# Kernel tuning notes

Hardware: AMD Instinct MI355X
Metric: run time of the kernel (lower is better)

The kernel has to match this reference:

```python
import jax, jax.numpy as jnp
import numpy as np

PI = float(np.pi)


def _make_grid(H, W, stride, k, delta):
    """Gnomonic (tangent-plane) sampling grid for one spherical conv layer.
    Returns rows (Ho, K) and cols (Ho, Wo, K) of fractional pixel coords."""
    Ho, Wo = H // stride, W // stride
    j = jnp.arange(k, dtype=jnp.float32) - (k - 1) / 2.0
    t = jnp.tan(delta / k * j)                      # tangent-plane tap coords
    yy = jnp.repeat(t, k)                           # (K,) vertical
    xx = jnp.tile(t, k)                             # (K,) horizontal
    rho = jnp.sqrt(xx ** 2 + yy ** 2)
    rho_s = jnp.where(rho == 0, 1.0, rho)
    nu = jnp.arctan(rho)
    # latitude of each output row center (equirect: row -> colatitude)
    lat0 = PI / 2 - (jnp.arange(Ho, dtype=jnp.float32) * stride + 0.5) * (PI / H)
    sl, cl = jnp.sin(lat0)[:, None], jnp.cos(lat0)[:, None]   # (Ho,1)
    sn, cn = jnp.sin(nu)[None, :], jnp.cos(nu)[None, :]       # (1,K)
    lat = jnp.arcsin(jnp.clip(cn * sl + (yy[None, :] / rho_s[None, :]) * sn * cl, -1.0, 1.0))
    dlon = jnp.arctan2(xx[None, :] * sn, rho[None, :] * cl * cn - yy[None, :] * sl * sn)
    rows = (PI / 2 - lat) / PI * H - 0.5            # (Ho,K) fractional row
    dcol = dlon / (2 * PI) * W                      # (Ho,K) longitude offset in px
    cols = (jnp.arange(Wo, dtype=jnp.float32) * stride)[None, :, None] + dcol[:, None, :]
    return rows, cols


def _bilinear(x, rows, cols):
    """x: (B,C,H,W); rows (Ho,K); cols (Ho,Wo,K). Latitude clamped, longitude wrapped.
    Returns patches (B,C,Ho,Wo,K)."""
    B, C, H, W = x.shape
    r0 = jnp.floor(rows); wr = (rows - r0)[:, None, :]
    c0 = jnp.floor(cols); wc = cols - c0
    r0i = jnp.clip(r0, 0, H - 1).astype(jnp.int32)
    r1i = jnp.clip(r0 + 1, 0, H - 1).astype(jnp.int32)
    c0i = jnp.mod(c0.astype(jnp.int32), W)
    c1i = jnp.mod(c0i + 1, W)

    def g(ri, ci):
        return x[:, :, ri[:, None, :], ci]          # (B,C,Ho,Wo,K)

    return (g(r0i, c0i) * (1 - wr) * (1 - wc) + g(r0i, c1i) * (1 - wr) * wc
            + g(r1i, c0i) * wr * (1 - wc) + g(r1i, c1i) * wr * wc)


def _sconv(x, w, b, delta, stride):
    k = int(round(np.sqrt(w.shape[-1])))
    rows, cols = _make_grid(x.shape[2], x.shape[3], stride, k, delta)
    p = _bilinear(x, rows, cols)                    # (B,C,Ho,Wo,K)
    return jnp.einsum('bchwk,ock->bohw', p, w) + b[None, :, None, None]


def _bn_relu(x, g, b):
    m = x.mean((0, 2, 3), keepdims=True)
    v = jnp.mean((x - m) ** 2, (0, 2, 3), keepdims=True)  # biased var (torch BN train)
    return jax.nn.relu((x - m) / jnp.sqrt(v + 1e-5) * g[None, :, None, None] + b[None, :, None, None])


def _up2(x):
    return jnp.repeat(jnp.repeat(x, 2, axis=2), 2, axis=3)


def _forward(input, w1, b1, g1, bb1, w2, b2, g2, bb2, w3, b3, g3, bb3,
             w31, b31, g31, bb31, w4, b4, g4, bb4, w41, b41, g41, bb41,
             w5, b5, g5, bb5, w6, b6, g6, bb6):
    x1 = _bn_relu(_sconv(input, w1, b1, PI / 32, 2), g1, bb1)
    x2 = _bn_relu(_sconv(x1, w2, b2, PI / 16, 2), g2, bb2)
    x3 = _bn_relu(_sconv(x2, w3, b3, PI / 4, 2), g3, bb3)
    x31 = _bn_relu(_sconv(x3, w31, b31, PI / 4, 1), g31, bb31)
    x4 = _bn_relu(_sconv(x31, w4, b4, PI / 2, 2), g4, bb4)
    x41 = _bn_relu(_sconv(x4, w41, b41, PI / 2, 1), g41, bb41)
    x5 = _bn_relu(_sconv(jnp.concatenate([_up2(x41), x31], 1), w5, b5, PI / 4, 1), g5, bb5)
    x6 = _bn_relu(_sconv(jnp.concatenate([_up2(x5), x2], 1), w6, b6, PI / 8, 1), g6, bb6)
    return x6


_CFGS = [('1', 32, 6, 7), ('2', 64, 32, 5), ('3', 128, 64, 5), ('31', 128, 128, 3),
         ('4', 256, 128, 3), ('41', 256, 256, 3), ('5', 256, 384, 3), ('6', 128, 320, 3)]


def setup_inputs() -> dict:
    key = jax.random.key(0)
    inp = {'input': jax.random.normal(jax.random.fold_in(key, 0), (4, 6, 256, 512), jnp.float32)}
    for i, (s, o, c, kk) in enumerate(_CFGS):
        kw = jax.random.fold_in(key, i + 1)
        inp['w' + s] = jax.random.normal(kw, (o, c, kk * kk), jnp.float32) / np.float32(np.sqrt(c * kk * kk))
        inp['b' + s] = jnp.zeros((o,), jnp.float32)
        inp['g' + s] = jnp.ones((o,), jnp.float32)
        inp['bb' + s] = jnp.zeros((o,), jnp.float32)
    return inp


def reference(input, w1, b1, g1, bb1, w2, b2, g2, bb2, w3, b3, g3, bb3,
              w31, b31, g31, bb31, w4, b4, g4, bb4, w41, b41, g41, bb41,
              w5, b5, g5, bb5, w6, b6, g6, bb6):
    return _forward(input, w1, b1, g1, bb1, w2, b2, g2, bb2, w3, b3, g3, bb3,
                    w31, b31, g31, bb31, w4, b4, g4, bb4, w41, b41, g41, bb41,
                    w5, b5, g5, bb5, w6, b6, g6, bb6)
```

## Files before the change

kernel.cpp:

```cpp
#include <hip/hip_runtime.h>
#include <cstddef>
#include <cstdint>

#define PI_F 3.14159265358979323846f

typedef __attribute__((ext_vector_type(8))) short short8;
typedef __attribute__((ext_vector_type(4))) float floatx4;

__device__ __forceinline__ short f2bf(float f) {
    union { float f; unsigned u; } v; v.f = f;
    unsigned r = v.u + 0x7FFFu + ((v.u >> 16) & 1u);
    return (short)(r >> 16);
}

__global__ __launch_bounds__(256) void wtrans_kernel(
    const float* __restrict__ A, short* __restrict__ Abf,
    int M, int Mpad, int K2, int C, int Cp, int Kp, int Korig)
{
    int idx = blockIdx.x * 256 + threadIdx.x;
    if (idx >= Mpad * Kp) return;
    int m = idx / Kp;
    int k = idx - m * Kp;
    int tap = (unsigned)k / (unsigned)Cp;
    int c   = k - tap * Cp;
    float v = 0.f;
    if (m < M && tap < K2 && c < C) v = A[(size_t)m * Korig + c * K2 + tap];
    Abf[idx] = f2bf(v);
}

__global__ __launch_bounds__(256) void zero_kernel(float* __restrict__ p, int n)
{
    int i = blockIdx.x * 256 + threadIdx.x;
    if (i < n) p[i] = 0.f;
}

__global__ __launch_bounds__(256) void zero3_kernel(
    float* __restrict__ a, int na, float* __restrict__ b, int nb,
    float* __restrict__ c, int nc)
{
    int i = blockIdx.x * 256 + threadIdx.x;
    if (i < na) { a[i] = 0.f; return; }
    i -= na;
    if (i < nb) { b[i] = 0.f; return; }
    i -= nb;
    if (i < nc) c[i] = 0.f;
}

#define BNT 64
#define BKT 32
#define LDK 40

template<int MW, int SK>
__global__ __launch_bounds__(256) void sconv_mfma_kernel(
    const short* __restrict__ Abf,
    const float* __restrict__ src1, const float* __restrict__ src2,
    float2* __restrict__ part, int nBlkN,
    int C1, int Ctot, int Cp, int H, int W, int up1,
    int K2, int ksz, int stride, int lWo, int lHo, float delta,
    float* __restrict__ Y, int M, int Kp, int N, int lgM)
{
    __shared__ short Bs[2][BNT][LDK];
    __shared__ float4 tab[64];

    constexpr int LGSK = (SK == 1) ? 0 : ((SK == 2) ? 1 : 2);

    const int tid = threadIdx.x;
    const int total = gridDim.x;
    const int pid = blockIdx.x;
    const int logical = (pid & 7) * (total >> 3) + (pid >> 3);
    const int mblk = logical & ((1 << lgM) - 1);
    const int rest = logical >> lgM;
    const int kslice = rest & (SK - 1);
    const int nblk = rest >> LGSK;
    const int m0 = mblk * (MW * 64);
    const int n0 = nblk * BNT;

    const int Wo  = 1 << lWo;
    const int Ho  = 1 << lHo;
    const int HW  = 1 << (lWo + lHo);

    const int nHo  = (lWo >= 6) ? 1 : (BNT >> lWo);
    const int nEnt = nHo * K2;
    const int hoBase = (n0 >> lWo) & (Ho - 1);
    if (tid < nEnt) {
        int hoL = tid / K2;
        int i   = tid - hoL * K2;
        int ho_g = hoBase + hoL;
        int jy = i / ksz, jx = i - jy * ksz;
        float halfk = (ksz - 1) * 0.5f;
        float yy = tanf(delta / (float)ksz * ((float)jy - halfk));
        float xx = tanf(delta / (float)ksz * ((float)jx - halfk));
        float rho = sqrtf(xx * xx + yy * yy);
        float rho_s = (rho == 0.f) ? 1.f : rho;
        float nu = atanf(rho);
        float lat0 = PI_F * 0.5f - ((float)(ho_g * stride) + 0.5f) * (PI_F / (float)H);
        float sl = sinf(lat0), cl = cosf(lat0);
        float sn = sinf(nu),  cn = cosf(nu);
        float arg = cn * sl + (yy / rho_s) * sn * cl;
        arg = fminf(1.f, fmaxf(-1.f, arg));
        float lat = asinf(arg);
        float dlon = atan2f(xx * sn, rho * cl * cn - yy * sl * sn);
        float row = (PI_F * 0.5f - lat) / PI_F * (float)H - 0.5f;
        float dcol = dlon / (2.f * PI_F) * (float)W;
        float r0f = floorf(row);
        float fr = row - r0f;
        int r0 = (int)r0f;
        int r0i = min(max(r0, 0), H - 1);
        int r1i = min(max(r0 + 1, 0), H - 1);
        tab[tid] = make_float4(fr, dcol, __int_as_float(r0i), __int_as_float(r1i));
    }

    const int nn    = tid & 63;
    const int kslot = tid >> 6;
    const int n_s  = n0 + nn;
    const int wo_s = n_s & (Wo - 1);
    const int hoL_s = nn >> lWo;
    const int b_s  = n_s >> (lWo + lHo);
    const int tabBase = hoL_s * K2;
    const float wo_px = (float)(wo_s * stride);
    const int Hs = H >> up1, Ws = W >> up1;
    const int plane1 = Hs * Ws;
    const int plane2 = H * W;
    const unsigned boff1 = (unsigned)__builtin_amdgcn_readfirstlane(
        (int)(b_s * C1 * plane1));
    const unsigned boff2 = (unsigned)__builtin_amdgcn_readfirstlane(
        (int)(b_s * (Ctot - C1) * plane2));

    const int Tper = (Kp / BKT) / SK;
    const int t0 = kslice * Tper;
    const bool smallC = (Cp < 32);
    int tap, cb;
    if (smallC) { tap = kslot; cb = 0; }
    else {
        int prog = t0 * BKT;
        tap = prog / Cp;
        cb  = prog - tap * Cp + kslot * 8;
    }
    const int dtap = smallC ? (32 / Cp) : 0;

    const int wave = tid >> 6;
    const int wrow = wave * (MW * 16);
    const int lane = tid & 63;
    const int l16  = lane & 15;
    const int quad = lane >> 4;

    const short* pA[MW];
#pragma unroll
    for (int i = 0; i < MW; i++)
        pA[i] = Abf + (size_t)(m0 + wrow + i * 16 + l16) * Kp + quad * 8;

    floatx4 acc[MW][4];
#pragma unroll
    for (int i = 0; i < MW; i++)
#pragma unroll
        for (int j = 0; j < 4; j++)
            acc[i][j] = (floatx4){0.f, 0.f, 0.f, 0.f};

    __syncthreads();

    for (int t = t0; t < t0 + Tper; t++) {
        const int k0 = t * BKT;
        const int buf = t & 1;
        const int tapS = __builtin_amdgcn_readfirstlane(tap);
        const int cbS  = __builtin_amdgcn_readfirstlane(cb);
        {
            const int tapc = min(tapS, K2 - 1);
            const float4 e = tab[tabBase + tapc];
            const float fr = e.x;
            const float col = wo_px + e.y;
            const int r0i = __float_as_int(e.z);
            const int r1i = __float_as_int(e.w);
            const float cf = floorf(col);
            const float fc = col - cf;
            const int c0 = ((int)cf) & (W - 1);
            const int c1 = (c0 + 1) & (W - 1);
            const float w00 = (1.f - fr) * (1.f - fc);
            const float w01 = (1.f - fr) * fc;
            const float w10 = fr * (1.f - fc);
            const float w11 = fr * fc;

            const char* sbase; unsigned o00, o01, o10, o11, planeB;
            if (cbS < C1) {
                const int ra = (r0i >> up1) * Ws, rb = (r1i >> up1) * Ws;
                const int ca = c0 >> up1, cx = c1 >> up1;
                const unsigned base = boff1 + (unsigned)cbS * (unsigned)plane1;
                o00 = (base + ra + ca) * 4u; o01 = (base + ra + cx) * 4u;
                o10 = (base + rb + ca) * 4u; o11 = (base + rb + cx) * 4u;
                planeB = (unsigned)plane1 * 4u; sbase = (const char*)src1;
            } else {
                const int ra = r0i * W, rb = r1i * W;
                const unsigned base = boff2 + (unsigned)(cbS - C1) * (unsigned)plane2;
                o00 = (base + ra + c0) * 4u; o01 = (base + ra + c1) * 4u;
                o10 = (base + rb + c0) * 4u; o11 = (base + rb + c1) * 4u;
                planeB = (unsigned)plane2 * 4u; sbase = (const char*)src2;
            }

            if (!smallC) {
                float q00[8], q01[8], q10[8], q11[8];
#pragma unroll
                for (int j = 0; j < 8; j++) {
                    q00[j] = *(const float*)(sbase + o00);
                    q01[j] = *(const float*)(sbase + o01);
                    q10[j] = *(const float*)(sbase + o10);
                    q11[j] = *(const float*)(sbase + o11);
                    o00 += planeB; o01 += planeB; o10 += planeB; o11 += planeB;
                }
                unsigned pk[4];
#pragma unroll
                for (int jj = 0; jj < 4; jj++) {
                    float v0 = w00 * q00[2 * jj]     + w01 * q01[2 * jj]
                             + w10 * q10[2 * jj]     + w11 * q11[2 * jj];
                    float v1 = w00 * q00[2 * jj + 1] + w01 * q01[2 * jj + 1]
                             + w10 * q10[2 * jj + 1] + w11 * q11[2 * jj + 1];
                    unsigned r;
                    asm("v_cvt_pk_bf16_f32 %0, %1, %2"
                        : "=v"(r) : "v"(v0), "v"(v1));
                    pk[jj] = r;
                }
                *(uint4*)&Bs[buf][nn][kslot * 8] =
                    make_uint4(pk[0], pk[1], pk[2], pk[3]);
            } else {
                short t8[8];
#pragma unroll
                for (int j = 0; j < 8; j++) {
                    float v = 0.f;
                    if (cbS + j < Ctot) {
                        v = w00 * *(const float*)(sbase + o00)
                          + w01 * *(const float*)(sbase + o01)
                          + w10 * *(const float*)(sbase + o10)
                          + w11 * *(const float*)(sbase + o11);
                    }
                    t8[j] = f2bf(v);
                    o00 += planeB; o01 += planeB; o10 += planeB; o11 += planeB;
                }
                *(short8*)&Bs[buf][nn][kslot * 8] = *(short8*)&t8[0];
            }
        }
        __syncthreads();

        short8 af[MW];
#pragma unroll
        for (int i = 0; i < MW; i++)
            af[i] = *(const short8*)(pA[i] + k0);
        short8 bf[4];
#pragma unroll
        for (int j = 0; j < 4; j++)
            bf[j] = *(const short8*)&Bs[buf][j * 16 + l16][quad * 8];
#pragma unroll
        for (int i = 0; i < MW; i++)
#pragma unroll
            for (int j = 0; j < 4; j++)
                acc[i][j] = __builtin_amdgcn_mfma_f32_16x16x32_bf16(
                    af[i], bf[j], acc[i][j], 0, 0, 0);

        if (smallC) { tap += dtap; }
        else { cb += 32; if (cb >= Cp) { cb -= Cp; tap++; } }
    }

    if (SK == 1) {
#pragma unroll
        for (int i = 0; i < MW; i++) {
#pragma unroll
            for (int rr = 0; rr < 4; rr++) {
                const int m = m0 + wrow + i * 16 + quad * 4 + rr;
                const bool mv = (m < M);
                float s = 0.f, q = 0.f;
#pragma unroll
                for (int j = 0; j < 4; j++) {
                    const int n = n0 + j * 16 + l16;
                    const float v = acc[i][j][rr];
                    s += v; q += v * v;
                    if (mv) {
                        const int wo = n & (Wo - 1);
                        const int r  = n >> lWo;
                        const int ho = r & (Ho - 1);
                        const int b_ = r >> lHo;
                        Y[((size_t)b_ * M + m) * HW + (ho << lWo) + wo] = v;
                    }
                }
#pragma unroll
                for (int mask = 1; mask < 16; mask <<= 1) {
                    s += __shfl_xor(s, mask);
                    q += __shfl_xor(q, mask);
                }
                if (mv && l16 == 0)
                    part[(size_t)m * nBlkN + nblk] = make_float2(s, q);
            }
        }
    } else {
#pragma unroll
        for (int i = 0; i < MW; i++) {
#pragma unroll
            for (int j = 0; j < 4; j++) {
                const int n = n0 + j * 16 + l16;
                const int wo = n & (Wo - 1);
                const int r  = n >> lWo;
                const int ho = r & (Ho - 1);
                const int b_ = r >> lHo;
#pragma unroll
                for (int rr = 0; rr < 4; rr++) {
                    const int m = m0 + wrow + i * 16 + quad * 4 + rr;
                    if (m < M)
                        unsafeAtomicAdd(
                            &Y[((size_t)b_ * M + m) * HW + (ho << lWo) + wo],
                            acc[i][j][rr]);
                }
            }
        }
    }
}

__global__ __launch_bounds__(256) void bn_stats8_kernel(
    const float* __restrict__ Y, float2* __restrict__ part,
    int Co, int HW, int B)
{
    int co = blockIdx.x;
    int sp = blockIdx.y;
    int tid = threadIdx.x;
    int Nt = B * HW;
    int len = Nt >> 3;
    int start = sp * len, end = start + len;
    float s = 0.f, q = 0.f;
    for (int idx = start + tid; idx < end; idx += 256) {
        int b = idx / HW; int o = idx - b * HW;
        float v = Y[((size_t)b * Co + co) * HW + o];
        s += v; q += v * v;
    }
    __shared__ float sh_s[256], sh_q[256];
    sh_s[tid] = s; sh_q[tid] = q;
    __syncthreads();
    for (int off = 128; off > 0; off >>= 1) {
        if (tid < off) { sh_s[tid] += sh_s[tid + off]; sh_q[tid] += sh_q[tid + off]; }
        __syncthreads();
    }
    if (tid == 0)
        part[co * 8 + sp] = make_float2(sh_s[0], sh_q[0]);
}

__global__ __launch_bounds__(256) void bn_finalize_kernel(
    const float2* __restrict__ part, float2* __restrict__ scSf,
    const float* __restrict__ g, const float* __restrict__ bb,
    int nBlkN, int Nt)
{
    int c = blockIdx.x;
    int tid = threadIdx.x;
    double s = 0.0, q = 0.0;
    for (int k = tid; k < nBlkN; k += 256) {
        float2 p = part[(size_t)c * nBlkN + k];
        s += p.x; q += p.y;
    }
    __shared__ double sh_s[256], sh_q[256];
    sh_s[tid] = s; sh_q[tid] = q;
    __syncthreads();
    for (int off = 128; off > 0; off >>= 1) {
        if (tid < off) { sh_s[tid] += sh_s[tid + off]; sh_q[tid] += sh_q[tid + off]; }
        __syncthreads();
    }
    if (tid == 0) {
        double mean = sh_s[0] / Nt;
        double var = sh_q[0] / Nt - mean * mean;
        if (var < 0.0) var = 0.0;
        float sc = g[c] / sqrtf((float)var + 1e-5f);
        scSf[c] = make_float2(sc, bb[c] - (float)mean * sc);
    }
}

__global__ __launch_bounds__(256) void bn_apply_kernel(
    float* __restrict__ Y, const float2* __restrict__ scSf,
    int Co, int HW, int total)
{
    int idx = blockIdx.x * 256 + threadIdx.x;
    if (idx >= total) return;
    int c = (idx / HW) % Co;
    float2 s = scSf[c];
    float v = Y[idx] * s.x + s.y;
    Y[idx] = v > 0.f ? v : 0.f;
}

__global__ __launch_bounds__(256) void bn_apply_sk_kernel(
    float* __restrict__ Y, const float2* __restrict__ part,
    const float* __restrict__ g, const float* __restrict__ bb,
    int Co, int HW, int Nt, int total)
{
    int idx = blockIdx.x * 256 + threadIdx.x;
    int c = (idx / HW) % Co;
    __shared__ float s_sc, s_sf;
    if (threadIdx.x == 0) {
        double s = 0.0, q = 0.0;
        for (int p = 0; p < 8; p++) {
            float2 pp = part[c * 8 + p];
            s += pp.x; q += pp.y;
        }
        double mean = s / Nt;
        double var = q / Nt - mean * mean;
        if (var < 0.0) var = 0.0;
        float sc = g[c] / sqrtf((float)var + 1e-5f);
        s_sc = sc;
        s_sf = bb[c] - (float)mean * sc;
    }
    __syncthreads();
    if (idx >= total) return;
    float v = Y[idx] * s_sc + s_sf;
    Y[idx] = v > 0.f ? v : 0.f;
}

extern "C" void kernel_launch(void* const* d_in, const int* in_sizes, int n_in,
                              void* d_out, int out_size, void* d_ws, size_t ws_size,
                              hipStream_t stream)
{
    const int B = 4;
    char* ws = (char*)d_ws;
    size_t off = 0;
    auto allocb = [&](size_t bytes) -> void* {
        void* p = ws + off;
        off = (off + bytes + 255) & ~(size_t)255;
        return p;
    };

    float2* part = (float2*)allocb((size_t)65536 * sizeof(float2));
    float2* scSf = (float2*)allocb(256 * sizeof(float2));
    float* x2  = (float*)allocb((size_t)B * 64  * 64 * 128 * 4);
    float* x31 = (float*)allocb((size_t)B * 128 * 32 * 64 * 4);
    float* Q   = (float*)allocb((size_t)B * 32  * 128 * 256 * 4);
    float* x1  = Q;
    float* x3  = Q;
    float* x4  = Q;
    float* x41 = Q + (size_t)B * 256 * 16 * 32;
    float* x5  = Q + 2 * (size_t)B * 256 * 16 * 32;

    static const int kH[8]  = {256, 128,  64,  32,  32,  16,  32,  64};
    static const int kW[8]  = {512, 256, 128,  64,  64,  32,  64, 128};
    static const int kK[8]  = {  7,   5,   5,   3,   3,   3,   3,   3};
    static const int kSt[8] = {  2,   2,   2,   1,   2,   1,   1,   1};
    static const int kC[8]  = {  6,  32,  64, 128, 128, 256, 384, 320};
    static const int kM[8]  = { 32,  64, 128, 128, 256, 256, 256, 128};
    static const int kMW[8] = {  1,   1,   1,   1,   1,   1,   2,   2};
    static const int kSK[8] = {  1,   2,   4,   4,   4,   4,   4,   2};

    int Cp_[8], Kp_[8], Mpad_[8];
    short* Abf[8];
    for (int i = 0; i < 8; i++) {
        int K2 = kK[i] * kK[i];
        int Cp = (kC[i] < 8) ? 8 : kC[i];
        int gran = 32 * kSK[i];
        int Kp = (K2 * Cp + gran - 1) / gran * gran;
        int Mpad = (kM[i] + 63) & ~63;
        Cp_[i] = Cp; Kp_[i] = Kp; Mpad_[i] = Mpad;
        Abf[i] = (short*)allocb((size_t)Mpad * Kp * sizeof(short));
    }
    (void)ws_size; (void)in_sizes; (void)n_in; (void)out_size;

    struct LCfg { const float *s1, *s2; int C1, up; float delta; int widx; float* Y; };
    const float* input = (const float*)d_in[0];
    LCfg L[8] = {
        { input, nullptr,   6, 0, PI_F / 32.f,  1, x1  },
        { x1,    nullptr,  32, 0, PI_F / 16.f,  5, x2  },
        { x2,    nullptr,  64, 0, PI_F / 4.f,   9, x3  },
        { x3,    nullptr, 128, 0, PI_F / 4.f,  13, x31 },
        { x31,   nullptr, 128, 0, PI_F / 2.f,  17, x4  },
        { x4,    nullptr, 256, 0, PI_F / 2.f,  21, x41 },
        { x41,   x31,     256, 1, PI_F / 4.f,  25, x5  },
        { x5,    x2,      256, 1, PI_F / 8.f,  29, (float*)d_out },
    };

    {
        int n_x2 = B * 64 * 64 * 128;
        int n_x31 = B * 128 * 32 * 64;
        int n_out = B * 128 * 64 * 128;
        int tot = n_x2 + n_x31 + n_out;
        zero3_kernel<<<dim3((tot + 255) / 256), dim3(256), 0, stream>>>(
            x2, n_x2, x31, n_x31, (float*)d_out, n_out);
    }

    for (int i = 0; i < 8; i++) {
        const LCfg& c = L[i];
        int H = kH[i], W = kW[i], k = kK[i], st = kSt[i];
        int Ho = H / st, Wo = W / st;
        int K2 = k * k;
        int C  = kC[i], M = kM[i];
        int HW = Ho * Wo;
        int N  = B * HW;
        int lWo = __builtin_ctz(Wo), lHo = __builtin_ctz(Ho);
        const float* Wt   = (const float*)d_in[c.widx];
        const float* gam  = (const float*)d_in[c.widx + 2];
        const float* bet  = (const float*)d_in[c.widx + 3];
        int total = B * M * HW;

        int tn = Mpad_[i] * Kp_[i];
        wtrans_kernel<<<dim3((tn + 255) / 256), dim3(256), 0, stream>>>(
            Wt, Abf[i], M, Mpad_[i], K2, C, Cp_[i], Kp_[i], C * K2);

        int MWi = kMW[i], SKi = kSK[i];
        int nBlkM = Mpad_[i] / (64 * MWi);
        int nBlkN = N / BNT;
        int totalBlk = nBlkN * nBlkM * SKi;
        int lgM = __builtin_ctz(nBlkM);

        if (SKi > 1 && i >= 2 && i <= 6 && c.Y != x31)
            zero_kernel<<<dim3((total + 255) / 256), dim3(256), 0, stream>>>(
                c.Y, total);

        #define CONV_ARGS Abf[i], c.s1, c.s2, part, nBlkN, \
            c.C1, C, Cp_[i], H, W, c.up, K2, k, st, lWo, lHo, c.delta, \
            c.Y, M, Kp_[i], N, lgM
        if      (MWi == 1 && SKi == 1)
            sconv_mfma_kernel<1,1><<<dim3(totalBlk), dim3(256), 0, stream>>>(CONV_ARGS);
        else if (MWi == 1 && SKi == 2)
            sconv_mfma_kernel<1,2><<<dim3(totalBlk), dim3(256), 0, stream>>>(CONV_ARGS);
        else if (MWi == 1 && SKi == 4)
            sconv_mfma_kernel<1,4><<<dim3(totalBlk), dim3(256), 0, stream>>>(CONV_ARGS);
        else if (MWi == 2 && SKi == 2)
            sconv_mfma_kernel<2,2><<<dim3(totalBlk), dim3(256), 0, stream>>>(CONV_ARGS);
        else
            sconv_mfma_kernel<2,4><<<dim3(totalBlk), dim3(256), 0, stream>>>(CONV_ARGS);
        #undef CONV_ARGS

        if (SKi > 1) {
            bn_stats8_kernel<<<dim3(M, 8), dim3(256), 0, stream>>>(
                c.Y, part, M, HW, B);
            bn_apply_sk_kernel<<<dim3(total / 256), dim3(256), 0, stream>>>(
                c.Y, part, gam, bet, M, HW, N, total);
        } else {
            bn_finalize_kernel<<<dim3(M), dim3(256), 0, stream>>>(
                part, scSf, gam, bet, nBlkN, N);
            bn_apply_kernel<<<dim3(total / 256), dim3(256), 0, stream>>>(
                c.Y, scSf, M, HW, total);
        }
    }
}
```

Measured before the change: 780.9 us.

## Stage source rows cooperatively into LDS via async global_load_lds for split-K convs

Adds a COOP variant of the spherical-conv MFMA kernel. The block first loads whole source rows for the current channel slice and tap into dynamic LDS using global_load_lds, then does the bilinear interpolation from LDS instead of issuing four scattered global loads per element. The next tile's rows and A fragments are prefetched while the current MFMAs run. This is meant to remove redundant, uncoalesced gather traffic. The cost is extra dynamic LDS, which can lower occupancy, plus a waitcnt/barrier on every iteration. The new path assumes power-of-two widths and that the source fits the staging layout.

After: 741.7 us. -5.0%, faster.

```diff
diff --git a/kernel.cpp b/kernel.cpp
--- a/kernel.cpp
+++ b/kernel.cpp
@@ -50,7 +50,7 @@
 #define BKT 32
 #define LDK 40
 
-template<int MW, int SK>
+template<int MW, int SK, bool COOP>
 __global__ __launch_bounds__(256) void sconv_mfma_kernel(
     const short* __restrict__ Abf,
     const float* __restrict__ src1, const float* __restrict__ src2,
@@ -61,6 +61,7 @@
 {
     __shared__ short Bs[2][BNT][LDK];
     __shared__ float4 tab[64];
+    extern __shared__ __align__(16) char dynLds[];
 
     constexpr int LGSK = (SK == 1) ? 0 : ((SK == 2) ? 1 : 2);
 
@@ -156,105 +157,241 @@
         for (int j = 0; j < 4; j++)
             acc[i][j] = (floatx4){0.f, 0.f, 0.f, 0.f};
 
-    __syncthreads();
-
-    for (int t = t0; t < t0 + Tper; t++) {
-        const int k0 = t * BKT;
-        const int buf = t & 1;
-        const int tapS = __builtin_amdgcn_readfirstlane(tap);
-        const int cbS  = __builtin_amdgcn_readfirstlane(cb);
+    if constexpr (!COOP) {
+        __syncthreads();
+
+        for (int t = t0; t < t0 + Tper; t++) {
+            const int k0 = t * BKT;
+            const int buf = t & 1;
+            const int tapS = __builtin_amdgcn_readfirstlane(tap);
+            const int cbS  = __builtin_amdgcn_readfirstlane(cb);
+            {
+                const int tapc = min(tapS, K2 - 1);
+                const float4 e = tab[tabBase + tapc];
+                const float fr = e.x;
+                const float col = wo_px + e.y;
+                const int r0i = __float_as_int(e.z);
+                const int r1i = __float_as_int(e.w);
+                const float cf = floorf(col);
+                const float fc = col - cf;
+                const int c0 = ((int)cf) & (W - 1);
+                const int c1 = (c0 + 1) & (W - 1);
+                const float w00 = (1.f - fr) * (1.f - fc);
+                const float w01 = (1.f - fr) * fc;
+                const float w10 = fr * (1.f - fc);
+                const float w11 = fr * fc;
+
+                const char* sbase; unsigned o00, o01, o10, o11, planeB;
+                if (cbS < C1) {
+                    const int ra = (r0i >> up1) * Ws, rb = (r1i >> up1) * Ws;
+                    const int ca = c0 >> up1, cx = c1 >> up1;
+                    const unsigned base = boff1 + (unsigned)cbS * (unsigned)plane1;
+                    o00 = (base + ra + ca) * 4u; o01 = (base + ra + cx) * 4u;
+                    o10 = (base + rb + ca) * 4u; o11 = (base + rb + cx) * 4u;
+                    planeB = (unsigned)plane1 * 4u; sbase = (const char*)src1;
+                } else {
+                    const int ra = r0i * W, rb = r1i * W;
+                    const unsigned base = boff2 + (unsigned)(cbS - C1) * (unsigned)plane2;
+                    o00 = (base + ra + c0) * 4u; o01 = (base + ra + c1) * 4u;
+                    o10 = (base + rb + c0) * 4u; o11 = (base + rb + c1) * 4u;
+                    planeB = (unsigned)plane2 * 4u; sbase = (const char*)src2;
+                }
+
+                if (!smallC) {
+                    float q00[8], q01[8], q10[8], q11[8];
+#pragma unroll
+                    for (int j = 0; j < 8; j++) {
+                        q00[j] = *(const float*)(sbase + o00);
+                        q01[j] = *(const float*)(sbase + o01);
+                        q10[j] = *(const float*)(sbase + o10);
+                        q11[j] = *(const float*)(sbase + o11);
+                        o00 += planeB; o01 += planeB; o10 += planeB; o11 += planeB;
+                    }
+                    unsigned pk[4];
+#pragma unroll
+                    for (int jj = 0; jj < 4; jj++) {
+                        float v0 = w00 * q00[2 * jj]     + w01 * q01[2 * jj]
+                                 + w10 * q10[2 * jj]     + w11 * q11[2 * jj];
+                        float v1 = w00 * q00[2 * jj + 1] + w01 * q01[2 * jj + 1]
+                                 + w10 * q10[2 * jj + 1] + w11 * q11[2 * jj + 1];
+                        unsigned r;
+                        asm("v_cvt_pk_bf16_f32 %0, %1, %2"
+                            : "=v"(r) : "v"(v0), "v"(v1));
+                        pk[jj] = r;
+                    }
+                    *(uint4*)&Bs[buf][nn][kslot * 8] =
+                        make_uint4(pk[0], pk[1], pk[2], pk[3]);
+                } else {
+                    short t8[8];
+#pragma unroll
+                    for (int j = 0; j < 8; j++) {
+                        float v = 0.f;
+                        if (cbS + j < Ctot) {
+                            v = w00 * *(const float*)(sbase + o00)
+                              + w01 * *(const float*)(sbase + o01)
+                              + w10 * *(const float*)(sbase + o10)
+                              + w11 * *(const float*)(sbase + o11);
+                        }
+                        t8[j] = f2bf(v);
+                        o00 += planeB; o01 += planeB; o10 += planeB; o11 += planeB;
+                    }
+                    *(short8*)&Bs[buf][nn][kslot * 8] = *(short8*)&t8[0];
+                }
+            }
+            __syncthreads();
+
+            short8 af[MW];
+#pragma unroll
+            for (int i = 0; i < MW; i++)
+                af[i] = *(const short8*)(pA[i] + k0);
+            short8 bfv[4];
+#pragma unroll
+            for (int j = 0; j < 4; j++)
+                bfv[j] = *(const short8*)&Bs[buf][j * 16 + l16][quad * 8];
+#pragma unroll
+            for (int i = 0; i < MW; i++)
+#pragma unroll
+                for (int j = 0; j < 4; j++)
+                    acc[i][j] = __builtin_amdgcn_mfma_f32_16x16x32_bf16(
+                        af[i], bfv[j], acc[i][j], 0, 0, 0);
+
+            if (smallC) { tap += dtap; }
+            else { cb += 32; if (cb >= Cp) { cb -= Cp; tap++; } }
+        }
+    } else {
+        const int lgW = __builtin_ctz(W);
+        const int lgWs1 = lgW - up1;
+        const int lgnHo = (nHo == 2) ? 1 : 0;
+        const int nHo2 = nHo << 1;
+        const int lg2nHo = lgnHo + 1;
+        const int NU = 64 * nHo;
+        const int kslotU = __builtin_amdgcn_readfirstlane(kslot);
+
+        auto stageTile = [&](int tapT, int cbT) {
+            const bool s1 = (cbT < C1);
+            const float* srcT = s1 ? src1 : src2;
+            const int lgWt = s1 ? lgWs1 : lgW;
+            const int upT  = s1 ? up1 : 0;
+            const int plT  = s1 ? plane1 : plane2;
+            const unsigned chB = s1
+                ? (boff1 + (unsigned)cbT * (unsigned)plane1)
+                : (boff2 + (unsigned)(cbT - C1) * (unsigned)plane2);
+            const int tapc2 = min(tapT, K2 - 1);
+            const int lgLPU = lgWt - 2;
+            const int NIw = (NU << lgWt) >> 10;
+            const int uW  = lane >> lgLPU;
+            const unsigned colB = (unsigned)(lane & ((1 << lgLPU) - 1)) << 2;
+            for (int ii = 0; ii < NIw; ii++) {
+                const int idx = kslotU * NIw + ii;
+                const int u = (idx << (6 - lgLPU)) + uW;
+                const int chL = u >> lg2nHo;
+                const int rem = u & (nHo2 - 1);
+                const int hoL = rem & (nHo - 1);
+                const float4 e = tab[hoL * K2 + tapc2];
+                const float rsel = (rem >> lgnHo) ? e.w : e.z;
+                const int r = __float_as_int(rsel) >> upT;
+                const float* gp = srcT + (chB + (unsigned)chL * (unsigned)plT
+                                          + ((unsigned)r << lgWt) + colB);
+                __builtin_amdgcn_global_load_lds(
+                    (const __attribute__((address_space(1))) void*)gp,
+                    (__attribute__((address_space(3))) void*)(dynLds + (size_t)idx * 1024),
+                    16, 0, 0);
+            }
+        };
+
+        int tapS, cb0S;
         {
-            const int tapc = min(tapS, K2 - 1);
-            const float4 e = tab[tabBase + tapc];
-            const float fr = e.x;
-            const float col = wo_px + e.y;
-            const int r0i = __float_as_int(e.z);
-            const int r1i = __float_as_int(e.w);
-            const float cf = floorf(col);
-            const float fc = col - cf;
-            const int c0 = ((int)cf) & (W - 1);
-            const int c1 = (c0 + 1) & (W - 1);
-            const float w00 = (1.f - fr) * (1.f - fc);
-            const float w01 = (1.f - fr) * fc;
-            const float w10 = fr * (1.f - fc);
-            const float w11 = fr * fc;
-
-            const char* sbase; unsigned o00, o01, o10, o11, planeB;
-            if (cbS < C1) {
-                const int ra = (r0i >> up1) * Ws, rb = (r1i >> up1) * Ws;
-                const int ca = c0 >> up1, cx = c1 >> up1;
-                const unsigned base = boff1 + (unsigned)cbS * (unsigned)plane1;
-                o00 = (base + ra + ca) * 4u; o01 = (base + ra + cx) * 4u;
-                o10 = (base + rb + ca) * 4u; o11 = (base + rb + cx) * 4u;
-                planeB = (unsigned)plane1 * 4u; sbase = (const char*)src1;
-            } else {
-                const int ra = r0i * W, rb = r1i * W;
-                const unsigned base = boff2 + (unsigned)(cbS - C1) * (unsigned)plane2;
-                o00 = (base + ra + c0) * 4u; o01 = (base + ra + c1) * 4u;
-                o10 = (base + rb + c0) * 4u; o11 = (base + rb + c1) * 4u;
-                planeB = (unsigned)plane2 * 4u; sbase = (const char*)src2;
-            }
-
-            if (!smallC) {
-                float q00[8], q01[8], q10[8], q11[8];
+            int prog = t0 * BKT;
+            tapS = prog / Cp;
+            cb0S = prog - tapS * Cp;
+        }
+
+        __syncthreads();
+
+        stageTile(tapS, cb0S);
+        short8 afc[MW];
+#pragma unroll
+        for (int i2 = 0; i2 < MW; i2++)
+            afc[i2] = *(const short8*)(pA[i2] + t0 * BKT);
+
+        for (int t = t0; t < t0 + Tper; t++) {
+            const int buf = t & 1;
+            tapS = __builtin_amdgcn_readfirstlane(tapS);
+            cb0S = __builtin_amdgcn_readfirstlane(cb0S);
+            const bool isS1 = (cb0S < C1);
+            const int lgWsrc = isS1 ? lgWs1 : lgW;
+            const int up1s   = isS1 ? up1 : 0;
+            const int tapcI  = min(tapS, K2 - 1);
+
+            asm volatile("s_waitcnt vmcnt(0)" ::: "memory");
+            __syncthreads();
+
+            {
+                const float4 e2 = tab[tabBase + tapcI];
+                const float fr = e2.x;
+                const float col = wo_px + e2.y;
+                const float cf = floorf(col);
+                const float fc = col - cf;
+                const int c0 = ((int)cf) & (W - 1);
+                const int c1 = (c0 + 1) & (W - 1);
+                const int c0s = c0 >> up1s, c1s = c1 >> up1s;
+                const float* rowsF = (const float*)dynLds;
+                unsigned b0 = (unsigned)((((kslot * 8) << lg2nHo) + hoL_s)) << lgWsrc;
+                const unsigned stepc = ((unsigned)nHo2 << lgWsrc);
+                const unsigned stepr = ((unsigned)nHo  << lgWsrc);
+                float vv[8];
 #pragma unroll
                 for (int j = 0; j < 8; j++) {
-                    q00[j] = *(const float*)(sbase + o00);
-                    q01[j] = *(const float*)(sbase + o01);
-                    q10[j] = *(const float*)(sbase + o10);
-                    q11[j] = *(const float*)(sbase + o11);
-                    o00 += planeB; o01 += planeB; o10 += planeB; o11 += planeB;
+                    const float x00 = rowsF[b0 + c0s];
+                    const float x01 = rowsF[b0 + c1s];
+                    const float x10 = rowsF[b0 + stepr + c0s];
+                    const float x11 = rowsF[b0 + stepr + c1s];
+                    const float h0 = x00 + fc * (x01 - x00);
+                    const float h1 = x10 + fc * (x11 - x10);
+                    vv[j] = h0 + fr * (h1 - h0);
+                    b0 += stepc;
                 }
                 unsigned pk[4];
 #pragma unroll
                 for (int jj = 0; jj < 4; jj++) {
-                    float v0 = w00 * q00[2 * jj]     + w01 * q01[2 * jj]
-                             + w10 * q10[2 * jj]     + w11 * q11[2 * jj];
-                    float v1 = w00 * q00[2 * jj + 1] + w01 * q01[2 * jj + 1]
-                             + w10 * q10[2 * jj + 1] + w11 * q11[2 * jj + 1];
-                    unsigned r;
+                    unsigned rr;
                     asm("v_cvt_pk_bf16_f32 %0, %1, %2"
-                        : "=v"(r) : "v"(v0), "v"(v1));
-                    pk[jj] = r;
+                        : "=v"(rr) : "v"(vv[2 * jj]), "v"(vv[2 * jj + 1]));
+                    pk[jj] = rr;
                 }
                 *(uint4*)&Bs[buf][nn][kslot * 8] =
                     make_uint4(pk[0], pk[1], pk[2], pk[3]);
-            } else {
-                short t8[8];
-#pragma unroll
-                for (int j = 0; j < 8; j++) {
-                    float v = 0.f;
-                    if (cbS + j < Ctot) {
-                        v = w00 * *(const float*)(sbase + o00)
-                          + w01 * *(const float*)(sbase + o01)
-                          + w10 * *(const float*)(sbase + o10)
-                          + w11 * *(const float*)(sbase + o11);
-                    }
-                    t8[j] = f2bf(v);
-                    o00 += planeB; o01 += planeB; o10 += planeB; o11 += planeB;
-                }
-                *(short8*)&Bs[buf][nn][kslot * 8] = *(short8*)&t8[0];
             }
-        }
-        __syncthreads();
-
-        short8 af[MW];
-#pragma unroll
-        for (int i = 0; i < MW; i++)
-            af[i] = *(const short8*)(pA[i] + k0);
-        short8 bf[4];
-#pragma unroll
-        for (int j = 0; j < 4; j++)
-            bf[j] = *(const short8*)&Bs[buf][j * 16 + l16][quad * 8];
-#pragma unroll
-        for (int i = 0; i < MW; i++)
+            __syncthreads();
+
+            int tapN = tapS, cbN = cb0S + BKT;
+            if (cbN >= Cp) { cbN = 0; tapN = tapS + 1; }
+            const bool more = (t + 1 < t0 + Tper);
+            short8 afn[MW];
+            if (more) {
+#pragma unroll
+                for (int i2 = 0; i2 < MW; i2++)
+                    afn[i2] = *(const short8*)(pA[i2] + (t + 1) * BKT);
+                stageTile(tapN, cbN);
+            }
+
+            short8 bfr[4];
 #pragma unroll
             for (int j = 0; j < 4; j++)
-                acc[i][j] = __builtin_amdgcn_mfma_f32_16x16x32_bf16(
-                    af[i], bf[j], acc[i][j], 0, 0, 0);
-
-        if (smallC) { tap += dtap; }
-        else { cb += 32; if (cb >= Cp) { cb -= Cp; tap++; } }
+                bfr[j] = *(const short8*)&Bs[buf][j * 16 + l16][quad * 8];
+#pragma unroll
+            for (int i2 = 0; i2 < MW; i2++)
+#pragma unroll
+                for (int j = 0; j < 4; j++)
+                    acc[i2][j] = __builtin_amdgcn_mfma_f32_16x16x32_bf16(
+                        afc[i2], bfr[j], acc[i2][j], 0, 0, 0);
+
+            tapS = tapN; cb0S = cbN;
+            if (more) {
+#pragma unroll
+                for (int i2 = 0; i2 < MW; i2++) afc[i2] = afn[i2];
+            }
+        }
     }
 
     if (SK == 1) {
@@ -496,6 +633,15 @@
         int totalBlk = nBlkN * nBlkM * SKi;
         int lgM = __builtin_ctz(nBlkM);
 
+        size_t dynB = 0;
+        if (i >= 2) {
+            int nHo_i = (Wo >= 64) ? 1 : (64 / Wo);
+            int w1 = W >> c.up;
+            int wmax = c.s2 ? W : w1;
+            if (w1 > wmax) wmax = w1;
+            dynB = (size_t)(64 * nHo_i) * (size_t)wmax * 4u;
+        }
+
         if (SKi > 1 && i >= 2 && i <= 6 && c.Y != x31)
             zero_kernel<<<dim3((total + 255) / 256), dim3(256), 0, stream>>>(
                 c.Y, total);
@@ -504,15 +650,15 @@
             c.C1, C, Cp_[i], H, W, c.up, K2, k, st, lWo, lHo, c.delta, \
             c.Y, M, Kp_[i], N, lgM
         if      (MWi == 1 && SKi == 1)
-            sconv_mfma_kernel<1,1><<<dim3(totalBlk), dim3(256), 0, stream>>>(CONV_ARGS);
+            sconv_mfma_kernel<1,1,false><<<dim3(totalBlk), dim3(256), 0, stream>>>(CONV_ARGS);
         else if (MWi == 1 && SKi == 2)
-            sconv_mfma_kernel<1,2><<<dim3(totalBlk), dim3(256), 0, stream>>>(CONV_ARGS);
+            sconv_mfma_kernel<1,2,false><<<dim3(totalBlk), dim3(256), 0, stream>>>(CONV_ARGS);
         else if (MWi == 1 && SKi == 4)
-            sconv_mfma_kernel<1,4><<<dim3(totalBlk), dim3(256), 0, stream>>>(CONV_ARGS);
+            sconv_mfma_kernel<1,4,true><<<dim3(totalBlk), dim3(256), dynB, stream>>>(CONV_ARGS);
         else if (MWi == 2 && SKi == 2)
-            sconv_mfma_kernel<2,2><<<dim3(totalBlk), dim3(256), 0, stream>>>(CONV_ARGS);
+            sconv_mfma_kernel<2,2,true><<<dim3(totalBlk), dim3(256), dynB, stream>>>(CONV_ARGS);
         else
-            sconv_mfma_kernel<2,4><<<dim3(totalBlk), dim3(256), 0, stream>>>(CONV_ARGS);
+            sconv_mfma_kernel<2,4,true><<<dim3(totalBlk), dim3(256), dynB, stream>>>(CONV_ARGS);
         #undef CONV_ARGS
 
         if (SKi > 1) {
```
